# Performance work log

Measured on AMD Instinct MI355X. Metric: run time of the kernel, lower is better.

## Reference

```python
import jax, jax.numpy as jnp
import numpy as np

B, N_REL, N_OBJ, N_ATT, VOCAB, D = 32, 1024, 1024, 4, 2048, 512


def setup_inputs() -> dict:
    key = jax.random.key(0)
    ks = jax.random.split(key, 12)
    inp = {}
    inp["ssg_rel"] = jax.random.randint(ks[0], (B, N_REL, 3), 0, N_OBJ, dtype=jnp.int32)
    inp["ssg_obj"] = jax.random.randint(ks[1], (B, N_OBJ), 0, VOCAB, dtype=jnp.int32)
    inp["ssg_att"] = jax.random.randint(ks[2], (B, N_OBJ, N_ATT), 0, VOCAB, dtype=jnp.int32)
    inp["emb_table"] = jax.random.normal(ks[3], (VOCAB, D), jnp.float32) * 0.02
    def lin(k, fan_in):
        return jax.random.normal(k, (fan_in, D), jnp.float32) * (1.0 / np.sqrt(fan_in))
    inp["W_sbj"] = lin(ks[4], 3 * D); inp["b_sbj"] = jnp.zeros((D,), jnp.float32)
    inp["W_obj"] = lin(ks[5], 3 * D); inp["b_obj"] = jnp.zeros((D,), jnp.float32)
    inp["W_rel"] = lin(ks[6], 3 * D); inp["b_rel"] = jnp.zeros((D,), jnp.float32)
    inp["W_o"] = lin(ks[7], D);      inp["b_o"] = jnp.zeros((D,), jnp.float32)
    inp["W_a"] = lin(ks[8], 2 * D);  inp["b_a"] = jnp.zeros((D,), jnp.float32)
    return inp


def reference(ssg_rel, ssg_obj, ssg_att, emb_table,
              W_sbj, b_sbj, W_obj, b_obj, W_rel, b_rel, W_o, b_o, W_a, b_a):
    # Dropout is identity in eval mode.
    Bq, N_rel, _ = ssg_rel.shape
    _, N_obj, N_att = ssg_att.shape
    d = emb_table.shape[1]

    rel_mask = (ssg_rel[:, :, 2] == 1)[..., None]      # [B, N_rel, 1], True = pad
    obj_mask = ssg_obj == 1                            # [B, N_obj]
    attr_mask = ssg_att == 1                           # [B, N_obj, N_att]

    rel_emb = emb_table[ssg_rel[:, :, 2]]              # [B, N_rel, d]
    obj_emb = emb_table[ssg_obj]                       # [B, N_obj, d]
    attr_emb = emb_table[ssg_att]                      # [B, N_obj, N_att, d]

    sbj_id = ssg_rel[:, :, 0]
    obj_id = ssg_rel[:, :, 1]
    gather = lambda ids: jnp.take_along_axis(obj_emb, ids[..., None], axis=1)  # [B,N_rel,d]
    sbj_g = gather(sbj_id)
    obj_g = gather(obj_id)

    zfill = lambda x: jnp.where(rel_mask, 0.0, x)
    # Sequential overwriting matches the original: rel_obj/rel_rel use the UPDATED sbj/obj feats.
    sbj_f = zfill(jax.nn.relu(jnp.concatenate([sbj_g, obj_g, rel_emb], -1) @ W_sbj + b_sbj))
    obj_f = zfill(jax.nn.relu(jnp.concatenate([sbj_f, obj_g, rel_emb], -1) @ W_obj + b_obj))
    rel_f = zfill(jax.nn.relu(jnp.concatenate([sbj_f, obj_f, rel_emb], -1) @ W_rel + b_rel))

    node = jnp.where(obj_mask[..., None], 0.0, jax.nn.relu(obj_emb @ W_o + b_o))  # [B,N_obj,d]

    att_in = jnp.concatenate(
        [jnp.broadcast_to(obj_emb[:, :, None, :], (Bq, N_obj, N_att, d)), attr_emb], -1)
    att_f = jnp.where(attr_mask[..., None], 0.0, jax.nn.relu(att_in @ W_a + b_a))  # [B,N_obj,N_att,d]

    bidx = jnp.arange(Bq)[:, None]
    node = node.at[bidx, sbj_id].add(sbj_f)
    node = node.at[bidx, obj_id].add(obj_f)

    # Original builds counts=ones(B, 2*N_rel, N_obj+1) then scatters 1s into it -> a no-op,
    # so counts.sum(dim=1) == 2*N_rel everywhere; the divisor is the constant 2*N_rel.
    rel_object_feat = node / jnp.asarray(2.0 * N_rel, node.dtype)

    att_sum = att_f.sum(axis=2)                        # [B, N_obj, d]
    att_cnt = jnp.sum(~attr_mask, axis=-1)             # [B, N_obj] number of valid attrs
    attr_zero = att_cnt == 0
    denom = jnp.maximum(att_cnt, 1).astype(att_sum.dtype)[..., None]
    att_feat = jnp.where(attr_zero[..., None], 0.0, att_sum / denom)

    ssg_feat = jnp.concatenate([rel_object_feat, rel_f, att_feat], axis=1)
    ssg_mask = jnp.concatenate([obj_mask, rel_mask[..., 0], attr_zero], axis=1)[:, None, None, :]
    return ssg_feat, ssg_mask
```

## Files before the change

kernel.cpp:

```cpp
#include <hip/hip_runtime.h>
#include <hip/hip_bf16.h>

typedef __attribute__((ext_vector_type(8))) short bf16x8;
typedef __attribute__((ext_vector_type(4))) float f32x4;

#define N_OBJ 1024
#define N_REL 1024
#define NB 32
#define D 512
#define VOCAB 2048
#define M_ROWS (NB * N_REL)
#define PRE_BLK (VOCAB * D)
#define WT_BLK (D * D)

__device__ __forceinline__ ushort f2bf(float f) {
    union { float f; unsigned u; } v; v.f = f;
    unsigned u = v.u;
    unsigned r = (u + 0x7FFFu + ((u >> 16) & 1u)) >> 16;
    return (ushort)r;
}
__device__ __forceinline__ float bf2f(ushort h) {
    union { unsigned u; float f; } v; v.u = ((unsigned)h) << 16;
    return v.f;
}

__device__ __forceinline__ void gload16(const ushort* g, const ushort* l) {
    __builtin_amdgcn_global_load_lds(
        (const __attribute__((address_space(1))) void*)(unsigned long long)(const void*)g,
        (__attribute__((address_space(3))) void*)(unsigned)(unsigned long long)(const void*)l,
        16, 0, 0);
}

__global__ void k_cvt_emb(const float* __restrict__ E, ushort* __restrict__ EB) {
    int i = blockIdx.x * 256 + threadIdx.x;
    float4 v = ((const float4*)E)[i];
    ushort4 o; o.x = f2bf(v.x); o.y = f2bf(v.y); o.z = f2bf(v.z); o.w = f2bf(v.w);
    ((ushort4*)EB)[i] = o;
}

__global__ void k_transpose_w(const float* __restrict__ Wsbj, const float* __restrict__ Wobj,
                              const float* __restrict__ Wrel, const float* __restrict__ Wo,
                              const float* __restrict__ Wa, ushort* __restrict__ WT) {
    __shared__ float s[32][33];
    int q = blockIdx.z;
    const float* src; int ro;
    if (q < 3)       { src = Wsbj; ro = q * 512; }
    else if (q < 6)  { src = Wobj; ro = (q - 3) * 512; }
    else if (q < 9)  { src = Wrel; ro = (q - 6) * 512; }
    else if (q == 9) { src = Wo;   ro = 0; }
    else             { src = Wa;   ro = (q - 10) * 512; }
    int tx = threadIdx.x, ty = threadIdx.y;
    int kbase = blockIdx.y * 32, nbase = blockIdx.x * 32;
#pragma unroll
    for (int i = 0; i < 4; i++) {
        int k = kbase + ty + i * 8;
        s[ty + i * 8][tx] = src[(size_t)(ro + k) * 512 + nbase + tx];
    }
    __syncthreads();
    ushort* dst = WT + (size_t)q * WT_BLK;
#pragma unroll
    for (int i = 0; i < 4; i++) {
        int n = nbase + ty + i * 8;
        dst[(size_t)n * 512 + kbase + tx] = f2bf(s[tx][ty + i * 8]);
    }
}

template <int MODE>
__global__ __launch_bounds__(256)
void k_gemm(const ushort* __restrict__ A, const ushort* __restrict__ WT,
            ushort* __restrict__ PREB,
            const int* __restrict__ ssg_rel, const int* __restrict__ ssg_obj,
            const float* __restrict__ bias,
            ushort* __restrict__ featbuf, float* __restrict__ out0,
            float* __restrict__ out1) {
    __shared__ __attribute__((aligned(16))) ushort sA[128 * 64];
    __shared__ __attribute__((aligned(16))) ushort sB[128 * 64];

    const int tid = threadIdx.x;
    int mt, nt;
    if (MODE == 0) { mt = blockIdx.x; nt = blockIdx.y; }
    else {
        int bid = blockIdx.y * 4 + blockIdx.x;
        int nb = (bid & 7) * 128 + (bid >> 3);
        mt = nb >> 2; nt = nb & 3;
    }
    const int m0 = mt * 128;
    constexpr int LDA = (MODE == 0) ? 512 : 1024;
    constexpr int KTOT = (MODE == 2) ? 1024 : 512;

    const ushort* BT0;
    const ushort* BT1 = nullptr;
    ushort* PREq = nullptr;
    if (MODE == 0) {
        const int wtq[9] = {0, 1, 2, 4, 5, 8, 9, 10, 11};
        int q = blockIdx.z;
        if ((q == 2 || q == 4 || q == 5) && mt >= 8) return;
        BT0 = WT + (size_t)wtq[q] * WT_BLK + (size_t)nt * 128 * 512;
        PREq = PREB + (size_t)q * PRE_BLK;
    } else if (MODE == 1) {
        BT0 = WT + (size_t)3 * WT_BLK + (size_t)nt * 128 * 512;
    } else {
        BT0 = WT + (size_t)6 * WT_BLK + (size_t)nt * 128 * 512;
        BT1 = WT + (size_t)7 * WT_BLK + (size_t)nt * 128 * 512;
    }

    const int wave = tid >> 6;
    const int wm = wave >> 1, wn = wave & 1;
    const int lr = tid & 15, lk = (tid & 63) >> 4;

    f32x4 acc[4][4];
#pragma unroll
    for (int mi = 0; mi < 4; mi++)
#pragma unroll
        for (int ni = 0; ni < 4; ni++)
            acc[mi][ni] = (f32x4){0.f, 0.f, 0.f, 0.f};

    const ushort* Ag = A + (size_t)m0 * LDA;
    const int srow = tid >> 3;
    const int scol = (tid & 7) * 8;

    for (int k0 = 0; k0 < KTOT; k0 += 64) {
        const ushort* As = Ag + (size_t)srow * LDA + k0 + scol;
        const ushort* Bbase = (MODE == 2 && k0 >= 512) ? (BT1 + (k0 - 512)) : (BT0 + k0);
        const ushort* Bs = Bbase + (size_t)srow * 512 + scol;
#pragma unroll
        for (int i = 0; i < 4; i++)
            gload16(As + (size_t)i * 32 * LDA, &sA[i * 2048 + tid * 8]);
#pragma unroll
        for (int i = 0; i < 4; i++)
            gload16(Bs + (size_t)i * 32 * 512, &sB[i * 2048 + tid * 8]);
        __syncthreads();
#pragma unroll
        for (int ks = 0; ks < 2; ks++) {
            bf16x8 af[4], bfr[4];
#pragma unroll
            for (int mi = 0; mi < 4; mi++)
                af[mi] = *(const bf16x8*)&sA[(wm * 64 + mi * 16 + lr) * 64 + ks * 32 + lk * 8];
#pragma unroll
            for (int ni = 0; ni < 4; ni++)
                bfr[ni] = *(const bf16x8*)&sB[(wn * 64 + ni * 16 + lr) * 64 + ks * 32 + lk * 8];
#pragma unroll
            for (int mi = 0; mi < 4; mi++)
#pragma unroll
                for (int ni = 0; ni < 4; ni++)
                    acc[mi][ni] = __builtin_amdgcn_mfma_f32_16x16x32_bf16(af[mi], bfr[ni], acc[mi][ni], 0, 0, 0);
        }
        __syncthreads();
    }

    int* sIo  = (int*)sA;
    int* sRid = sIo + 128;
    if (MODE == 1 || MODE == 2) {
        if (tid < 128) {
            int R = m0 + tid;
            int rid = ssg_rel[R * 3 + 2];
            sRid[tid] = rid;
            if (MODE == 1) sIo[tid] = ssg_obj[(R & ~(N_OBJ - 1)) + ssg_rel[R * 3 + 1]];
            if (MODE == 2 && nt == 0) {
                int b = R >> 10, rr = R & (N_REL - 1);
                out1[(size_t)b * 3072 + 1024 + rr] = (rid == 1) ? 1.0f : 0.0f;
            }
        }
        __syncthreads();
    }

#pragma unroll
    for (int mi = 0; mi < 4; mi++) {
#pragma unroll
        for (int ni = 0; ni < 4; ni++) {
            int c = wn * 64 + ni * 16 + lr;
            int ch = nt * 128 + c;
#pragma unroll
            for (int j = 0; j < 4; j++) {
                int rl = wm * 64 + mi * 16 + lk * 4 + j;
                int R = m0 + rl;
                float v = acc[mi][ni][j];
                if (MODE == 0) {
                    PREq[(size_t)R * 512 + ch] = f2bf(v);
                } else if (MODE == 1) {
                    int rid = sRid[rl];
                    int io = sIo[rl];
                    float t = v + bf2f(PREB[(size_t)3 * PRE_BLK + (size_t)io * 512 + ch])
                                + bf2f(PREB[(size_t)4 * PRE_BLK + (size_t)rid * 512 + ch])
                                + bias[ch];
                    t = fmaxf(t, 0.f);
                    if (rid == 1) t = 0.f;
                    featbuf[(size_t)R * 1024 + 512 + ch] = f2bf(t);
                } else {
                    int rid = sRid[rl];
                    float t = v + bf2f(PREB[(size_t)5 * PRE_BLK + (size_t)rid * 512 + ch])
                                + bias[ch];
                    t = fmaxf(t, 0.f);
                    if (rid == 1) t = 0.f;
                    int b = R >> 10, rr = R & (N_REL - 1);
                    out0[((size_t)(b * 3072 + 1024 + rr)) * 512 + ch] = t;
                }
            }
        }
    }
}

__global__ void k_sbj(const int* __restrict__ ssg_rel, const int* __restrict__ ssg_obj,
                      const ushort* __restrict__ PREB, const float* __restrict__ b_sbj,
                      ushort* __restrict__ featbuf) {
    int R = blockIdx.x * 2 + (threadIdx.x >> 7);
    int c4 = threadIdx.x & 127;
    int sid = ssg_rel[R * 3 + 0];
    int oid = ssg_rel[R * 3 + 1];
    int rid = ssg_rel[R * 3 + 2];
    int bb = R & ~(N_OBJ - 1);
    int is_ = ssg_obj[bb + sid];
    int io  = ssg_obj[bb + oid];
    ushort4 p1 = ((const ushort4*)(PREB + (size_t)is_ * 512))[c4];
    ushort4 p2 = ((const ushort4*)(PREB + (size_t)1 * PRE_BLK + (size_t)io * 512))[c4];
    ushort4 p3 = ((const ushort4*)(PREB + (size_t)2 * PRE_BLK + (size_t)rid * 512))[c4];
    float4 b  = ((const float4*)b_sbj)[c4];
    float4 v;
    v.x = fmaxf(bf2f(p1.x) + bf2f(p2.x) + bf2f(p3.x) + b.x, 0.f);
    v.y = fmaxf(bf2f(p1.y) + bf2f(p2.y) + bf2f(p3.y) + b.y, 0.f);
    v.z = fmaxf(bf2f(p1.z) + bf2f(p2.z) + bf2f(p3.z) + b.z, 0.f);
    v.w = fmaxf(bf2f(p1.w) + bf2f(p2.w) + bf2f(p3.w) + b.w, 0.f);
    if (rid == 1) { v.x = v.y = v.z = v.w = 0.f; }
    ushort4 o; o.x = f2bf(v.x); o.y = f2bf(v.y); o.z = f2bf(v.z); o.w = f2bf(v.w);
    *(ushort4*)&featbuf[(size_t)R * 1024 + c4 * 4] = o;
}

__global__ void k_zero(int* __restrict__ p) {
    p[blockIdx.x * 256 + threadIdx.x] = 0;
}
__global__ void k_csr_count(const int* __restrict__ ssg_rel, int* __restrict__ cnt) {
    int r = blockIdx.x * 256 + threadIdx.x;
    int bb = r & ~(N_OBJ - 1);
    atomicAdd(&cnt[bb + ssg_rel[r * 3 + 0]], 1);
    atomicAdd(&cnt[bb + ssg_rel[r * 3 + 1]], 1);
}
__global__ __launch_bounds__(1024)
void k_csr_scan(const int* __restrict__ cnt, int* __restrict__ offs, int* __restrict__ cursor) {
    __shared__ int part[1024];
    int t = threadIdx.x;
    int base = t * 32;
    int local[32];
    int sum = 0;
#pragma unroll
    for (int i = 0; i < 32; i++) { local[i] = sum; sum += cnt[base + i]; }
    part[t] = sum;
    __syncthreads();
    for (int d = 1; d < 1024; d <<= 1) {
        int v = (t >= d) ? part[t - d] : 0;
        __syncthreads();
        part[t] += v;
        __syncthreads();
    }
    int excl = (t == 0) ? 0 : part[t - 1];
#pragma unroll
    for (int i = 0; i < 32; i++) {
        int o = excl + local[i];
        offs[base + i] = o;
        cursor[base + i] = o;
    }
    if (t == 1023) offs[32768] = part[1023];
}
__global__ void k_csr_fill(const int* __restrict__ ssg_rel, int* __restrict__ cursor,
                           int* __restrict__ lists) {
    int r = blockIdx.x * 256 + threadIdx.x;
    int bb = r & ~(N_OBJ - 1);
    int p0 = atomicAdd(&cursor[bb + ssg_rel[r * 3 + 0]], 1);
    lists[p0] = r * 2;
    int p1 = atomicAdd(&cursor[bb + ssg_rel[r * 3 + 1]], 1);
    lists[p1] = r * 2 + 1;
}

__global__ void k_objpass(const int* __restrict__ ssg_obj, const int* __restrict__ ssg_att,
                          const int* __restrict__ offs, const int* __restrict__ lists,
                          const ushort* __restrict__ feat, const ushort* __restrict__ PREB,
                          const float* __restrict__ b_o, const float* __restrict__ b_a,
                          float* __restrict__ out0, float* __restrict__ out1) {
    int Ro = blockIdx.x * 2 + (threadIdx.x >> 7);
    int c4 = threadIdx.x & 127;
    int iv = ssg_obj[Ro];
    int bq = Ro >> 10, o = Ro & (N_OBJ - 1);

    float4 bo4 = ((const float4*)b_o)[c4];
    ushort4 q6 = ((const ushort4*)(PREB + (size_t)6 * PRE_BLK + (size_t)iv * 512))[c4];
    float a0 = 0.f, a1 = 0.f, a2 = 0.f, a3 = 0.f;
    if (iv != 1) {
        a0 = fmaxf(bf2f(q6.x) + bo4.x, 0.f);
        a1 = fmaxf(bf2f(q6.y) + bo4.y, 0.f);
        a2 = fmaxf(bf2f(q6.z) + bo4.z, 0.f);
        a3 = fmaxf(bf2f(q6.w) + bo4.w, 0.f);
    }
    int s = offs[Ro], e = offs[Ro + 1];
    for (int i = s; i < e; ++i) {
        int ent = lists[i];
        ushort4 u = ((const ushort4*)(feat + (size_t)(ent >> 1) * 1024 + (ent & 1) * 512))[c4];
        a0 += bf2f(u.x); a1 += bf2f(u.y); a2 += bf2f(u.z); a3 += bf2f(u.w);
    }
    float4 r;
    r.x = a0 * (1.0f / 2048.0f); r.y = a1 * (1.0f / 2048.0f);
    r.z = a2 * (1.0f / 2048.0f); r.w = a3 * (1.0f / 2048.0f);
    ((float4*)out0)[((size_t)(bq * 3072 + o)) * 128 + c4] = r;

    int j0 = ssg_att[Ro * 4 + 0], j1 = ssg_att[Ro * 4 + 1];
    int j2 = ssg_att[Ro * 4 + 2], j3 = ssg_att[Ro * 4 + 3];
    float4 ba4 = ((const float4*)b_a)[c4];
    ushort4 q7 = ((const ushort4*)(PREB + (size_t)7 * PRE_BLK + (size_t)iv * 512))[c4];
    float bx = bf2f(q7.x) + ba4.x, by = bf2f(q7.y) + ba4.y;
    float bz = bf2f(q7.z) + ba4.z, bw = bf2f(q7.w) + ba4.w;
    int cnt = (j0 != 1) + (j1 != 1) + (j2 != 1) + (j3 != 1);
    float inv = cnt ? 1.0f / (float)cnt : 0.f;
    float sx = 0.f, sy = 0.f, sz = 0.f, sw = 0.f;
    const ushort* A2 = PREB + (size_t)8 * PRE_BLK;
#define ACC_ATT(J) if ((J) != 1) { \
        ushort4 a2 = ((const ushort4*)(A2 + (size_t)(J) * 512))[c4]; \
        sx += fmaxf(bx + bf2f(a2.x), 0.f); sy += fmaxf(by + bf2f(a2.y), 0.f); \
        sz += fmaxf(bz + bf2f(a2.z), 0.f); sw += fmaxf(bw + bf2f(a2.w), 0.f); }
    ACC_ATT(j0) ACC_ATT(j1) ACC_ATT(j2) ACC_ATT(j3)
#undef ACC_ATT
    float4 sv; sv.x = sx * inv; sv.y = sy * inv; sv.z = sz * inv; sv.w = sw * inv;
    ((float4*)out0)[((size_t)(bq * 3072 + 2048 + o)) * 128 + c4] = sv;

    if (c4 == 0) {
        out1[(size_t)bq * 3072 + o] = (iv == 1) ? 1.0f : 0.0f;
        out1[(size_t)bq * 3072 + 2048 + o] = (cnt == 0) ? 1.0f : 0.0f;
    }
}

extern "C" void kernel_launch(void* const* d_in, const int* in_sizes, int n_in,
                              void* d_out, int out_size, void* d_ws, size_t ws_size,
                              hipStream_t stream) {
    const int*   ssg_rel = (const int*)d_in[0];
    const int*   ssg_obj = (const int*)d_in[1];
    const int*   ssg_att = (const int*)d_in[2];
    const float* emb     = (const float*)d_in[3];
    const float* Wsbj    = (const float*)d_in[4];
    const float* bsbj    = (const float*)d_in[5];
    const float* Wobj    = (const float*)d_in[6];
    const float* bobj    = (const float*)d_in[7];
    const float* Wrel    = (const float*)d_in[8];
    const float* brel    = (const float*)d_in[9];
    const float* Wo      = (const float*)d_in[10];
    const float* bo      = (const float*)d_in[11];
    const float* Wa      = (const float*)d_in[12];
    const float* ba      = (const float*)d_in[13];

    float* out0 = (float*)d_out;
    float* out1 = out0 + (size_t)NB * 3072 * 512;

    char* w = (char*)d_ws;
    ushort* EB     = (ushort*)w; w += (size_t)VOCAB * D * 2;
    ushort* WT     = (ushort*)w; w += (size_t)12 * WT_BLK * 2;
    ushort* PREB   = (ushort*)w; w += (size_t)9 * PRE_BLK * 2;
    ushort* feat   = (ushort*)w; w += (size_t)M_ROWS * 1024 * 2;
    int*    cnt    = (int*)   w; w += (size_t)32768 * 4;
    int*    offs   = (int*)   w; w += (size_t)32769 * 4;
    int*    cursor = (int*)   w; w += (size_t)32768 * 4;
    int*    lists  = (int*)   w; w += (size_t)65536 * 4;

    k_cvt_emb<<<dim3(VOCAB * D / 1024), dim3(256), 0, stream>>>(emb, EB);
    k_transpose_w<<<dim3(16, 16, 12), dim3(32, 8), 0, stream>>>(Wsbj, Wobj, Wrel, Wo, Wa, WT);
    k_zero<<<dim3(128), dim3(256), 0, stream>>>(cnt);
    k_csr_count<<<dim3(128), dim3(256), 0, stream>>>(ssg_rel, cnt);
    k_csr_scan<<<dim3(1), dim3(1024), 0, stream>>>(cnt, offs, cursor);
    k_csr_fill<<<dim3(128), dim3(256), 0, stream>>>(ssg_rel, cursor, lists);
    k_gemm<0><<<dim3(16, 4, 9), dim3(256), 0, stream>>>(EB, WT, PREB, ssg_rel, ssg_obj,
                                                        nullptr, nullptr, nullptr, nullptr);
    k_sbj<<<dim3(M_ROWS / 2), dim3(256), 0, stream>>>(ssg_rel, ssg_obj, PREB, bsbj, feat);
    k_gemm<1><<<dim3(4, M_ROWS / 128), dim3(256), 0, stream>>>(feat, WT, PREB, ssg_rel, ssg_obj,
                                                               bobj, feat, nullptr, nullptr);
    k_gemm<2><<<dim3(4, M_ROWS / 128), dim3(256), 0, stream>>>(feat, WT, PREB, ssg_rel, ssg_obj,
                                                               brel, nullptr, out0, out1);
    k_objpass<<<dim3(M_ROWS / 2), dim3(256), 0, stream>>>(ssg_obj, ssg_att, offs, lists,
                                                          feat, PREB, bo, ba, out0, out1);
}
```

Before: 237.6 us.

## Merge independent kernels into heterogeneous launches to cut launch count and tail idle

Fuses embedding conversion, weight transposes and count zeroing into one setup kernel, co-launches the CSR fill with the precompute GEMM, and splits the object pass so attribute averaging runs alongside the mode-1 GEMM and node aggregation runs alongside the mode-2 GEMM. This is meant to reduce kernel launch overhead and fill idle CUs during GEMM tails by mixing independent work. The risk is that shared-memory allocation for the GEMM branch now applies to every block, which can lower occupancy for the elementwise blocks. Imbalanced block types may also schedule poorly.

```diff
diff --git a/kernel.cpp b/kernel.cpp
--- a/kernel.cpp
+++ b/kernel.cpp
@@ -31,59 +31,16 @@
         16, 0, 0);
 }
 
-__global__ void k_cvt_emb(const float* __restrict__ E, ushort* __restrict__ EB) {
-    int i = blockIdx.x * 256 + threadIdx.x;
-    float4 v = ((const float4*)E)[i];
-    ushort4 o; o.x = f2bf(v.x); o.y = f2bf(v.y); o.z = f2bf(v.z); o.w = f2bf(v.w);
-    ((ushort4*)EB)[i] = o;
-}
-
-__global__ void k_transpose_w(const float* __restrict__ Wsbj, const float* __restrict__ Wobj,
-                              const float* __restrict__ Wrel, const float* __restrict__ Wo,
-                              const float* __restrict__ Wa, ushort* __restrict__ WT) {
-    __shared__ float s[32][33];
-    int q = blockIdx.z;
-    const float* src; int ro;
-    if (q < 3)       { src = Wsbj; ro = q * 512; }
-    else if (q < 6)  { src = Wobj; ro = (q - 3) * 512; }
-    else if (q < 9)  { src = Wrel; ro = (q - 6) * 512; }
-    else if (q == 9) { src = Wo;   ro = 0; }
-    else             { src = Wa;   ro = (q - 10) * 512; }
-    int tx = threadIdx.x, ty = threadIdx.y;
-    int kbase = blockIdx.y * 32, nbase = blockIdx.x * 32;
-#pragma unroll
-    for (int i = 0; i < 4; i++) {
-        int k = kbase + ty + i * 8;
-        s[ty + i * 8][tx] = src[(size_t)(ro + k) * 512 + nbase + tx];
-    }
-    __syncthreads();
-    ushort* dst = WT + (size_t)q * WT_BLK;
-#pragma unroll
-    for (int i = 0; i < 4; i++) {
-        int n = nbase + ty + i * 8;
-        dst[(size_t)n * 512 + kbase + tx] = f2bf(s[tx][ty + i * 8]);
-    }
-}
-
 template <int MODE>
-__global__ __launch_bounds__(256)
-void k_gemm(const ushort* __restrict__ A, const ushort* __restrict__ WT,
-            ushort* __restrict__ PREB,
-            const int* __restrict__ ssg_rel, const int* __restrict__ ssg_obj,
-            const float* __restrict__ bias,
-            ushort* __restrict__ featbuf, float* __restrict__ out0,
-            float* __restrict__ out1) {
-    __shared__ __attribute__((aligned(16))) ushort sA[128 * 64];
-    __shared__ __attribute__((aligned(16))) ushort sB[128 * 64];
-
-    const int tid = threadIdx.x;
-    int mt, nt;
-    if (MODE == 0) { mt = blockIdx.x; nt = blockIdx.y; }
-    else {
-        int bid = blockIdx.y * 4 + blockIdx.x;
-        int nb = (bid & 7) * 128 + (bid >> 3);
-        mt = nb >> 2; nt = nb & 3;
-    }
+__device__ __forceinline__ void gemm_body(
+    int mt, int nt, int q, int tid,
+    ushort* __restrict__ sA, ushort* __restrict__ sB,
+    const ushort* __restrict__ A, const ushort* __restrict__ WT,
+    ushort* __restrict__ PREB,
+    const int* __restrict__ ssg_rel, const int* __restrict__ ssg_obj,
+    const float* __restrict__ bias,
+    ushort* __restrict__ featbuf, float* __restrict__ out0,
+    float* __restrict__ out1) {
     const int m0 = mt * 128;
     constexpr int LDA = (MODE == 0) ? 512 : 1024;
     constexpr int KTOT = (MODE == 2) ? 1024 : 512;
@@ -93,8 +50,6 @@
     ushort* PREq = nullptr;
     if (MODE == 0) {
         const int wtq[9] = {0, 1, 2, 4, 5, 8, 9, 10, 11};
-        int q = blockIdx.z;
-        if ((q == 2 || q == 4 || q == 5) && mt >= 8) return;
         BT0 = WT + (size_t)wtq[q] * WT_BLK + (size_t)nt * 128 * 512;
         PREq = PREB + (size_t)q * PRE_BLK;
     } else if (MODE == 1) {
@@ -200,6 +155,162 @@
     }
 }
 
+__device__ __forceinline__ void att_body(
+    int Ro, int c4, const int* __restrict__ ssg_obj, const int* __restrict__ ssg_att,
+    const ushort* __restrict__ PREB, const float* __restrict__ b_a,
+    float* __restrict__ out0, float* __restrict__ out1) {
+    int iv = ssg_obj[Ro];
+    int bq = Ro >> 10, o = Ro & (N_OBJ - 1);
+    int j0 = ssg_att[Ro * 4 + 0], j1 = ssg_att[Ro * 4 + 1];
+    int j2 = ssg_att[Ro * 4 + 2], j3 = ssg_att[Ro * 4 + 3];
+    float4 ba4 = ((const float4*)b_a)[c4];
+    ushort4 q7 = ((const ushort4*)(PREB + (size_t)7 * PRE_BLK + (size_t)iv * 512))[c4];
+    float bx = bf2f(q7.x) + ba4.x, by = bf2f(q7.y) + ba4.y;
+    float bz = bf2f(q7.z) + ba4.z, bw = bf2f(q7.w) + ba4.w;
+    int cnt = (j0 != 1) + (j1 != 1) + (j2 != 1) + (j3 != 1);
+    float inv = cnt ? 1.0f / (float)cnt : 0.f;
+    float sx = 0.f, sy = 0.f, sz = 0.f, sw = 0.f;
+    const ushort* A2 = PREB + (size_t)8 * PRE_BLK;
+#define ACC_ATT(J) if ((J) != 1) { \
+        ushort4 a2 = ((const ushort4*)(A2 + (size_t)(J) * 512))[c4]; \
+        sx += fmaxf(bx + bf2f(a2.x), 0.f); sy += fmaxf(by + bf2f(a2.y), 0.f); \
+        sz += fmaxf(bz + bf2f(a2.z), 0.f); sw += fmaxf(bw + bf2f(a2.w), 0.f); }
+    ACC_ATT(j0) ACC_ATT(j1) ACC_ATT(j2) ACC_ATT(j3)
+#undef ACC_ATT
+    float4 sv; sv.x = sx * inv; sv.y = sy * inv; sv.z = sz * inv; sv.w = sw * inv;
+    ((float4*)out0)[((size_t)(bq * 3072 + 2048 + o)) * 128 + c4] = sv;
+    if (c4 == 0) {
+        out1[(size_t)bq * 3072 + o] = (iv == 1) ? 1.0f : 0.0f;
+        out1[(size_t)bq * 3072 + 2048 + o] = (cnt == 0) ? 1.0f : 0.0f;
+    }
+}
+
+__device__ __forceinline__ void node_body(
+    int Ro, int c4, const int* __restrict__ ssg_obj,
+    const int* __restrict__ offs, const int* __restrict__ lists,
+    const ushort* __restrict__ feat, const ushort* __restrict__ PREB,
+    const float* __restrict__ b_o, float* __restrict__ out0) {
+    int iv = ssg_obj[Ro];
+    int bq = Ro >> 10, o = Ro & (N_OBJ - 1);
+    float4 bo4 = ((const float4*)b_o)[c4];
+    ushort4 q6 = ((const ushort4*)(PREB + (size_t)6 * PRE_BLK + (size_t)iv * 512))[c4];
+    float a0 = 0.f, a1 = 0.f, a2 = 0.f, a3 = 0.f;
+    if (iv != 1) {
+        a0 = fmaxf(bf2f(q6.x) + bo4.x, 0.f);
+        a1 = fmaxf(bf2f(q6.y) + bo4.y, 0.f);
+        a2 = fmaxf(bf2f(q6.z) + bo4.z, 0.f);
+        a3 = fmaxf(bf2f(q6.w) + bo4.w, 0.f);
+    }
+    int s = offs[Ro], e = offs[Ro + 1];
+    for (int i = s; i < e; ++i) {
+        int ent = lists[i];
+        ushort4 u = ((const ushort4*)(feat + (size_t)(ent >> 1) * 1024 + (ent & 1) * 512))[c4];
+        a0 += bf2f(u.x); a1 += bf2f(u.y); a2 += bf2f(u.z); a3 += bf2f(u.w);
+    }
+    float4 r;
+    r.x = a0 * (1.0f / 2048.0f); r.y = a1 * (1.0f / 2048.0f);
+    r.z = a2 * (1.0f / 2048.0f); r.w = a3 * (1.0f / 2048.0f);
+    ((float4*)out0)[((size_t)(bq * 3072 + o)) * 128 + c4] = r;
+}
+
+__global__ __launch_bounds__(256)
+void k_setup(const float* __restrict__ E, ushort* __restrict__ EB,
+             const float* __restrict__ Wsbj, const float* __restrict__ Wobj,
+             const float* __restrict__ Wrel, const float* __restrict__ Wo,
+             const float* __restrict__ Wa, ushort* __restrict__ WT,
+             int* __restrict__ cnt) {
+    int blk = blockIdx.x, tid = threadIdx.x;
+    if (blk < 1024) {
+        int i = blk * 256 + tid;
+        float4 v = ((const float4*)E)[i];
+        ushort4 o; o.x = f2bf(v.x); o.y = f2bf(v.y); o.z = f2bf(v.z); o.w = f2bf(v.w);
+        ((ushort4*)EB)[i] = o;
+    } else if (blk < 4096) {
+        __shared__ float s[32][33];
+        int bb = blk - 1024;
+        int q = bb >> 8, rem = bb & 255;
+        int bx = rem & 15, by = rem >> 4;
+        const float* src; int ro;
+        if (q < 3)       { src = Wsbj; ro = q * 512; }
+        else if (q < 6)  { src = Wobj; ro = (q - 3) * 512; }
+        else if (q < 9)  { src = Wrel; ro = (q - 6) * 512; }
+        else if (q == 9) { src = Wo;   ro = 0; }
+        else             { src = Wa;   ro = (q - 10) * 512; }
+        int tx = tid & 31, ty = tid >> 5;
+        int kbase = by * 32, nbase = bx * 32;
+#pragma unroll
+        for (int i = 0; i < 4; i++) {
+            int k = kbase + ty + i * 8;
+            s[ty + i * 8][tx] = src[(size_t)(ro + k) * 512 + nbase + tx];
+        }
+        __syncthreads();
+        ushort* dst = WT + (size_t)q * WT_BLK;
+#pragma unroll
+        for (int i = 0; i < 4; i++) {
+            int n = nbase + ty + i * 8;
+            dst[(size_t)n * 512 + kbase + tx] = f2bf(s[tx][ty + i * 8]);
+        }
+    } else {
+        cnt[(blk - 4096) * 256 + tid] = 0;
+    }
+}
+
+__global__ void k_csr_count(const int* __restrict__ ssg_rel, int* __restrict__ cnt) {
+    int r = blockIdx.x * 256 + threadIdx.x;
+    int bb = r & ~(N_OBJ - 1);
+    atomicAdd(&cnt[bb + ssg_rel[r * 3 + 0]], 1);
+    atomicAdd(&cnt[bb + ssg_rel[r * 3 + 1]], 1);
+}
+
+__global__ __launch_bounds__(1024)
+void k_csr_scan(const int* __restrict__ cnt, int* __restrict__ offs, int* __restrict__ cursor) {
+    __shared__ int part[1024];
+    int t = threadIdx.x;
+    int base = t * 32;
+    int local[32];
+    int sum = 0;
+#pragma unroll
+    for (int i = 0; i < 32; i++) { local[i] = sum; sum += cnt[base + i]; }
+    part[t] = sum;
+    __syncthreads();
+    for (int d = 1; d < 1024; d <<= 1) {
+        int v = (t >= d) ? part[t - d] : 0;
+        __syncthreads();
+        part[t] += v;
+        __syncthreads();
+    }
+    int excl = (t == 0) ? 0 : part[t - 1];
+#pragma unroll
+    for (int i = 0; i < 32; i++) {
+        int o = excl + local[i];
+        offs[base + i] = o;
+        cursor[base + i] = o;
+    }
+    if (t == 1023) offs[32768] = part[1023];
+}
+
+__global__ __launch_bounds__(256)
+void k_pre_fill(const ushort* __restrict__ EB, const ushort* __restrict__ WT,
+                ushort* __restrict__ PREB, const int* __restrict__ ssg_rel,
+                int* __restrict__ cursor, int* __restrict__ lists) {
+    int blk = blockIdx.x, tid = threadIdx.x;
+    if (blk < 576) {
+        int q = blk >> 6, mt = (blk >> 2) & 15, nt = blk & 3;
+        if ((q == 2 || q == 4 || q == 5) && mt >= 8) return;
+        __shared__ __attribute__((aligned(16))) ushort sA[128 * 64];
+        __shared__ __attribute__((aligned(16))) ushort sB[128 * 64];
+        gemm_body<0>(mt, nt, q, tid, sA, sB, EB, WT, PREB,
+                     nullptr, nullptr, nullptr, nullptr, nullptr, nullptr);
+    } else {
+        int r = (blk - 576) * 256 + tid;
+        int bb = r & ~(N_OBJ - 1);
+        int p0 = atomicAdd(&cursor[bb + ssg_rel[r * 3 + 0]], 1);
+        lists[p0] = r * 2;
+        int p1 = atomicAdd(&cursor[bb + ssg_rel[r * 3 + 1]], 1);
+        lists[p1] = r * 2 + 1;
+    }
+}
+
 __global__ void k_sbj(const int* __restrict__ ssg_rel, const int* __restrict__ ssg_obj,
                       const ushort* __restrict__ PREB, const float* __restrict__ b_sbj,
                       ushort* __restrict__ featbuf) {
@@ -225,103 +336,46 @@
     *(ushort4*)&featbuf[(size_t)R * 1024 + c4 * 4] = o;
 }
 
-__global__ void k_zero(int* __restrict__ p) {
-    p[blockIdx.x * 256 + threadIdx.x] = 0;
-}
-__global__ void k_csr_count(const int* __restrict__ ssg_rel, int* __restrict__ cnt) {
-    int r = blockIdx.x * 256 + threadIdx.x;
-    int bb = r & ~(N_OBJ - 1);
-    atomicAdd(&cnt[bb + ssg_rel[r * 3 + 0]], 1);
-    atomicAdd(&cnt[bb + ssg_rel[r * 3 + 1]], 1);
-}
-__global__ __launch_bounds__(1024)
-void k_csr_scan(const int* __restrict__ cnt, int* __restrict__ offs, int* __restrict__ cursor) {
-    __shared__ int part[1024];
-    int t = threadIdx.x;
-    int base = t * 32;
-    int local[32];
-    int sum = 0;
-#pragma unroll
-    for (int i = 0; i < 32; i++) { local[i] = sum; sum += cnt[base + i]; }
-    part[t] = sum;
-    __syncthreads();
-    for (int d = 1; d < 1024; d <<= 1) {
-        int v = (t >= d) ? part[t - d] : 0;
-        __syncthreads();
-        part[t] += v;
-        __syncthreads();
-    }
-    int excl = (t == 0) ? 0 : part[t - 1];
-#pragma unroll
-    for (int i = 0; i < 32; i++) {
-        int o = excl + local[i];
-        offs[base + i] = o;
-        cursor[base + i] = o;
-    }
-    if (t == 1023) offs[32768] = part[1023];
-}
-__global__ void k_csr_fill(const int* __restrict__ ssg_rel, int* __restrict__ cursor,
-                           int* __restrict__ lists) {
-    int r = blockIdx.x * 256 + threadIdx.x;
-    int bb = r & ~(N_OBJ - 1);
-    int p0 = atomicAdd(&cursor[bb + ssg_rel[r * 3 + 0]], 1);
-    lists[p0] = r * 2;
-    int p1 = atomicAdd(&cursor[bb + ssg_rel[r * 3 + 1]], 1);
-    lists[p1] = r * 2 + 1;
-}
-
-__global__ void k_objpass(const int* __restrict__ ssg_obj, const int* __restrict__ ssg_att,
-                          const int* __restrict__ offs, const int* __restrict__ lists,
-                          const ushort* __restrict__ feat, const ushort* __restrict__ PREB,
-                          const float* __restrict__ b_o, const float* __restrict__ b_a,
-                          float* __restrict__ out0, float* __restrict__ out1) {
-    int Ro = blockIdx.x * 2 + (threadIdx.x >> 7);
-    int c4 = threadIdx.x & 127;
-    int iv = ssg_obj[Ro];
-    int bq = Ro >> 10, o = Ro & (N_OBJ - 1);
-
-    float4 bo4 = ((const float4*)b_o)[c4];
-    ushort4 q6 = ((const ushort4*)(PREB + (size_t)6 * PRE_BLK + (size_t)iv * 512))[c4];
-    float a0 = 0.f, a1 = 0.f, a2 = 0.f, a3 = 0.f;
-    if (iv != 1) {
-        a0 = fmaxf(bf2f(q6.x) + bo4.x, 0.f);
-        a1 = fmaxf(bf2f(q6.y) + bo4.y, 0.f);
-        a2 = fmaxf(bf2f(q6.z) + bo4.z, 0.f);
-        a3 = fmaxf(bf2f(q6.w) + bo4.w, 0.f);
-    }
-    int s = offs[Ro], e = offs[Ro + 1];
-    for (int i = s; i < e; ++i) {
-        int ent = lists[i];
-        ushort4 u = ((const ushort4*)(feat + (size_t)(ent >> 1) * 1024 + (ent & 1) * 512))[c4];
-        a0 += bf2f(u.x); a1 += bf2f(u.y); a2 += bf2f(u.z); a3 += bf2f(u.w);
-    }
-    float4 r;
-    r.x = a0 * (1.0f / 2048.0f); r.y = a1 * (1.0f / 2048.0f);
-    r.z = a2 * (1.0f / 2048.0f); r.w = a3 * (1.0f / 2048.0f);
-    ((float4*)out0)[((size_t)(bq * 3072 + o)) * 128 + c4] = r;
-
-    int j0 = ssg_att[Ro * 4 + 0], j1 = ssg_att[Ro * 4 + 1];
-    int j2 = ssg_att[Ro * 4 + 2], j3 = ssg_att[Ro * 4 + 3];
-    float4 ba4 = ((const float4*)b_a)[c4];
-    ushort4 q7 = ((const ushort4*)(PREB + (size_t)7 * PRE_BLK + (size_t)iv * 512))[c4];
-    float bx = bf2f(q7.x) + ba4.x, by = bf2f(q7.y) + ba4.y;
-    float bz = bf2f(q7.z) + ba4.z, bw = bf2f(q7.w) + ba4.w;
-    int cnt = (j0 != 1) + (j1 != 1) + (j2 != 1) + (j3 != 1);
-    float inv = cnt ? 1.0f / (float)cnt : 0.f;
-    float sx = 0.f, sy = 0.f, sz = 0.f, sw = 0.f;
-    const ushort* A2 = PREB + (size_t)8 * PRE_BLK;
-#define ACC_ATT(J) if ((J) != 1) { \
-        ushort4 a2 = ((const ushort4*)(A2 + (size_t)(J) * 512))[c4]; \
-        sx += fmaxf(bx + bf2f(a2.x), 0.f); sy += fmaxf(by + bf2f(a2.y), 0.f); \
-        sz += fmaxf(bz + bf2f(a2.z), 0.f); sw += fmaxf(bw + bf2f(a2.w), 0.f); }
-    ACC_ATT(j0) ACC_ATT(j1) ACC_ATT(j2) ACC_ATT(j3)
-#undef ACC_ATT
-    float4 sv; sv.x = sx * inv; sv.y = sy * inv; sv.z = sz * inv; sv.w = sw * inv;
-    ((float4*)out0)[((size_t)(bq * 3072 + 2048 + o)) * 128 + c4] = sv;
-
-    if (c4 == 0) {
-        out1[(size_t)bq * 3072 + o] = (iv == 1) ? 1.0f : 0.0f;
-        out1[(size_t)bq * 3072 + 2048 + o] = (cnt == 0) ? 1.0f : 0.0f;
+__global__ __launch_bounds__(256)
+void k_mode1_att(const ushort* __restrict__ feat, const ushort* __restrict__ WT,
+                 ushort* __restrict__ PREB,
+                 const int* __restrict__ ssg_rel, const int* __restrict__ ssg_obj,
+                 const int* __restrict__ ssg_att,
+                 const float* __restrict__ b_obj, const float* __restrict__ b_a,
+                 ushort* __restrict__ featbuf,
+                 float* __restrict__ out0, float* __restrict__ out1) {
+    int blk = blockIdx.x, tid = threadIdx.x;
+    if (blk < 1024) {
+        int nb = (blk & 7) * 128 + (blk >> 3);
+        int mt = nb >> 2, nt = nb & 3;
+        __shared__ __attribute__((aligned(16))) ushort sA[128 * 64];
+        __shared__ __attribute__((aligned(16))) ushort sB[128 * 64];
+        gemm_body<1>(mt, nt, 0, tid, sA, sB, feat, WT, PREB,
+                     ssg_rel, ssg_obj, b_obj, featbuf, nullptr, nullptr);
+    } else {
+        int Ro = (blk - 1024) * 2 + (tid >> 7);
+        att_body(Ro, tid & 127, ssg_obj, ssg_att, PREB, b_a, out0, out1);
+    }
+}
+
+__global__ __launch_bounds__(256)
+void k_mode2_node(const ushort* __restrict__ feat, const ushort* __restrict__ WT,
+                  ushort* __restrict__ PREB,
+                  const int* __restrict__ ssg_rel, const int* __restrict__ ssg_obj,
+                  const int* __restrict__ offs, const int* __restrict__ lists,
+                  const float* __restrict__ b_rel, const float* __restrict__ b_o,
+                  float* __restrict__ out0, float* __restrict__ out1) {
+    int blk = blockIdx.x, tid = threadIdx.x;
+    if (blk < 1024) {
+        int nb = (blk & 7) * 128 + (blk >> 3);
+        int mt = nb >> 2, nt = nb & 3;
+        __shared__ __attribute__((aligned(16))) ushort sA[128 * 64];
+        __shared__ __attribute__((aligned(16))) ushort sB[128 * 64];
+        gemm_body<2>(mt, nt, 0, tid, sA, sB, feat, WT, PREB,
+                     ssg_rel, ssg_obj, b_rel, nullptr, out0, out1);
+    } else {
+        int Ro = (blk - 1024) * 2 + (tid >> 7);
+        node_body(Ro, tid & 127, ssg_obj, offs, lists, feat, PREB, b_o, out0);
     }
 }
 
@@ -356,19 +410,13 @@
     int*    cursor = (int*)   w; w += (size_t)32768 * 4;
     int*    lists  = (int*)   w; w += (size_t)65536 * 4;
 
-    k_cvt_emb<<<dim3(VOCAB * D / 1024), dim3(256), 0, stream>>>(emb, EB);
-    k_transpose_w<<<dim3(16, 16, 12), dim3(32, 8), 0, stream>>>(Wsbj, Wobj, Wrel, Wo, Wa, WT);
-    k_zero<<<dim3(128), dim3(256), 0, stream>>>(cnt);
+    k_setup<<<dim3(4224), dim3(256), 0, stream>>>(emb, EB, Wsbj, Wobj, Wrel, Wo, Wa, WT, cnt);
     k_csr_count<<<dim3(128), dim3(256), 0, stream>>>(ssg_rel, cnt);
     k_csr_scan<<<dim3(1), dim3(1024), 0, stream>>>(cnt, offs, cursor);
-    k_csr_fill<<<dim3(128), dim3(256), 0, stream>>>(ssg_rel, cursor, lists);
-    k_gemm<0><<<dim3(16, 4, 9), dim3(256), 0, stream>>>(EB, WT, PREB, ssg_rel, ssg_obj,
-                                                        nullptr, nullptr, nullptr, nullptr);
+    k_pre_fill<<<dim3(704), dim3(256), 0, stream>>>(EB, WT, PREB, ssg_rel, cursor, lists);
     k_sbj<<<dim3(M_ROWS / 2), dim3(256), 0, stream>>>(ssg_rel, ssg_obj, PREB, bsbj, feat);
-    k_gemm<1><<<dim3(4, M_ROWS / 128), dim3(256), 0, stream>>>(feat, WT, PREB, ssg_rel, ssg_obj,
-                                                               bobj, feat, nullptr, nullptr);
-    k_gemm<2><<<dim3(4, M_ROWS / 128), dim3(256), 0, stream>>>(feat, WT, PREB, ssg_rel, ssg_obj,
-                                                               brel, nullptr, out0, out1);
-    k_objpass<<<dim3(M_ROWS / 2), dim3(256), 0, stream>>>(ssg_obj, ssg_att, offs, lists,
-                                                          feat, PREB, bo, ba, out0, out1);
-}
+    k_mode1_att<<<dim3(1024 + M_ROWS / 2), dim3(256), 0, stream>>>(
+        feat, WT, PREB, ssg_rel, ssg_obj, ssg_att, bobj, ba, feat, out0, out1);
+    k_mode2_node<<<dim3(1024 + M_ROWS / 2), dim3(256), 0, stream>>>(
+        feat, WT, PREB, ssg_rel, ssg_obj, offs, lists, brel, bo, out0, out1);
+}
```

After: 310.8 us. +30.8%, slower.
